# Optimization experiments

Measured on AMD Instinct MI355X. Metric: run time of the kernel, lower is better.

The kernel has to match this reference:

```python
import jax, jax.numpy as jnp
import numpy as np

N_NODES = 50000
N_EDGES = 600000
IN_DIM = 128
HID = 64
HEADS = 4
NEG_SLOPE = 0.2


def _glorot(key, shape):
    fan_in, fan_out = shape[0], shape[-1]
    lim = jnp.sqrt(6.0 / (fan_in + fan_out))
    return jax.random.uniform(key, shape, jnp.float32, -lim, lim)


def setup_inputs() -> dict:
    key = jax.random.key(0)
    ks = jax.random.split(key, 16)
    x = jax.random.normal(ks[0], (N_NODES, IN_DIM), jnp.float32)
    edge_index = jax.random.randint(ks[1], (2, N_EDGES), 0, N_NODES, jnp.int32)
    # GAT layer 1: in=128 -> heads=4, out=64, concat -> 256
    W1 = _glorot(ks[2], (IN_DIM, HEADS * HID))
    a_src1 = _glorot(ks[3], (HEADS, HID))
    a_dst1 = _glorot(ks[4], (HEADS, HID))
    b1 = jnp.zeros((HEADS * HID,), jnp.float32)
    # GAT layer 2: in=256 -> heads=1, out=64, no concat
    W2 = _glorot(ks[5], (HEADS * HID, 1 * HID))
    a_src2 = _glorot(ks[6], (1, HID))
    a_dst2 = _glorot(ks[7], (1, HID))
    b2 = jnp.zeros((HID,), jnp.float32)
    # classifier: Linear(64,32) -> ReLU -> Dropout(eval: identity) -> Linear(32,2)
    Wc1 = _glorot(ks[8], (HID, 32))
    bc1 = jnp.zeros((32,), jnp.float32)
    Wc2 = _glorot(ks[9], (32, 2))
    bc2 = jnp.zeros((2,), jnp.float32)
    return {"x": x, "edge_index": edge_index,
            "W1": W1, "a_src1": a_src1, "a_dst1": a_dst1, "b1": b1,
            "W2": W2, "a_src2": a_src2, "a_dst2": a_dst2, "b2": b2,
            "Wc1": Wc1, "bc1": bc1, "Wc2": Wc2, "bc2": bc2}


def _gat_conv(x, src, dst, W, a_src, a_dst, b, heads, out_ch, concat):
    N = x.shape[0]
    h = (x @ W).reshape(N, heads, out_ch)          # [N,H,C]
    alpha_s = jnp.sum(h * a_src, axis=-1)          # [N,H]
    alpha_d = jnp.sum(h * a_dst, axis=-1)          # [N,H]
    e = jax.nn.leaky_relu(alpha_s[src] + alpha_d[dst], NEG_SLOPE)  # [E,H]
    # segment softmax over edges grouped by destination node
    m = jax.ops.segment_max(e, dst, num_segments=N)                # [N,H]
    ex = jnp.exp(e - m[dst])
    denom = jax.ops.segment_sum(ex, dst, num_segments=N)           # [N,H]
    alpha = ex / (denom[dst] + 1e-16)                              # [E,H]
    msg = h[src] * alpha[:, :, None]                               # [E,H,C]
    out = jax.ops.segment_sum(msg, dst, num_segments=N)            # [N,H,C]
    out = out.reshape(N, heads * out_ch) if concat else out.mean(axis=1)
    return out + b


def reference(x, edge_index, W1, a_src1, a_dst1, b1, W2, a_src2, a_dst2, b2,
              Wc1, bc1, Wc2, bc2):
    N = x.shape[0]
    # PyG GATConv default add_self_loops=True (same augmented edge set both layers)
    loops = jnp.arange(N, dtype=edge_index.dtype)
    src = jnp.concatenate([edge_index[0], loops])
    dst = jnp.concatenate([edge_index[1], loops])
    h = _gat_conv(x, src, dst, W1, a_src1, a_dst1, b1, HEADS, HID, True)
    h = jax.nn.relu(h)
    h = _gat_conv(h, src, dst, W2, a_src2, a_dst2, b2, 1, HID, False)
    h = jax.nn.relu(h)
    h = jax.nn.relu(h @ Wc1 + bc1)   # Dropout(0.2) is identity in eval mode
    return h @ Wc2 + bc2
```

## Files before the change

kernel.cpp:

```cpp
#include <hip/hip_runtime.h>
#include <hip/hip_fp16.h>

#define N_NODES 50000
#define N_EDGESx 600000
#define E_TOT   (N_EDGESx + N_NODES)
#define NEG_SLOPE 0.2f

typedef _Float16 f16x4 __attribute__((ext_vector_type(4)));
typedef float f32x4 __attribute__((ext_vector_type(4)));

__device__ __forceinline__ float lrelu(float x) { return x > 0.f ? x : NEG_SLOPE * x; }

__global__ __launch_bounds__(256) void count_k(const int* __restrict__ ei,
                                               int* __restrict__ counts) {
    int i = blockIdx.x * 256 + threadIdx.x;
    if (i >= E_TOT) return;
    int dst = (i < N_EDGESx) ? ei[N_EDGESx + i] : (i - N_EDGESx);
    atomicAdd(&counts[dst], 1);
}

__global__ __launch_bounds__(1024) void scanA(const int* __restrict__ counts,
                                              int* __restrict__ offs,
                                              int* __restrict__ chunks, int N) {
    __shared__ int sdata[1024];
    int t = threadIdx.x;
    int g = blockIdx.x * 1024 + t;
    int v = (g < N) ? counts[g] : 0;
    sdata[t] = v;
    __syncthreads();
    for (int off = 1; off < 1024; off <<= 1) {
        int x = (t >= off) ? sdata[t - off] : 0;
        __syncthreads();
        sdata[t] += x;
        __syncthreads();
    }
    int incl = sdata[t];
    if (g < N) offs[g] = incl - v;
    if (t == 1023) chunks[blockIdx.x] = incl;
}

__global__ void scanB(int* chunks, int nch) {
    int lane = threadIdx.x & 63;
    int orig = (lane < nch) ? chunks[lane] : 0;
    int v = orig;
#pragma unroll
    for (int off = 1; off < 64; off <<= 1) {
        int u = __shfl_up(v, off);
        if (lane >= off) v += u;
    }
    if (lane < nch) chunks[lane] = v - orig;
}

__global__ __launch_bounds__(1024) void scanC(int* __restrict__ offs,
                                              const int* __restrict__ chunks, int N) {
    int g = blockIdx.x * 1024 + threadIdx.x;
    if (g < N) offs[g] += chunks[blockIdx.x];
}

__global__ __launch_bounds__(256) void scatter_k(const int* __restrict__ ei,
                                                 const int* __restrict__ offs,
                                                 int* __restrict__ cursor,
                                                 int* __restrict__ edge_src) {
    int i = blockIdx.x * 256 + threadIdx.x;
    if (i >= E_TOT) return;
    int src, dst;
    if (i < N_EDGESx) { src = ei[i]; dst = ei[N_EDGESx + i]; }
    else              { src = dst = i - N_EDGESx; }
    int pos = atomicAdd(&cursor[dst], 1);
    edge_src[offs[dst] + pos] = src;
}

__global__ __launch_bounds__(256) void prepBoth_k(const float* __restrict__ W1,
                                                  const float* __restrict__ W2,
                                                  _Float16* __restrict__ Bt1,
                                                  _Float16* __restrict__ Bt2) {
    int b = blockIdx.x;
    if (b < 32) {
        constexpr int K = 128, N = 256;
        int q = b * 256 + threadIdx.x;
        int n = q & (N - 1);
        int k4 = q / N;
        f16x4 v;
#pragma unroll
        for (int i = 0; i < 4; ++i)
            v[i] = (_Float16)W1[(size_t)(k4 * 4 + i) * N + n];
        int idx = n * K + (((k4 >> 1) ^ (n & 15)) << 3) + ((k4 & 1) << 2);
        *(f16x4*)&Bt1[idx] = v;
    } else {
        constexpr int K = 256, N = 64;
        int q = (b - 32) * 256 + threadIdx.x;
        int n = q & (N - 1);
        int k4 = q / N;
        f16x4 v;
#pragma unroll
        for (int i = 0; i < 4; ++i) {
            int kg = k4 * 4 + i;
            int krow = (kg & 3) * 64 + (kg >> 2);
            v[i] = (_Float16)W2[(size_t)krow * N + n];
        }
        int idx = n * K + (((k4 >> 1) ^ (n & 15)) << 3) + ((k4 & 1) << 2);
        *(f16x4*)&Bt2[idx] = v;
    }
}

template<int K, int N, int CPW, typename AT, int CPERM, int ALPHA>
__global__ __launch_bounds__(256, 2) void gemm_mfma(const AT* __restrict__ A,
                                                    const _Float16* __restrict__ Bt,
                                                    _Float16* __restrict__ C,
                                                    const float* __restrict__ asrc,
                                                    const float* __restrict__ adst,
                                                    float* __restrict__ as_o,
                                                    float* __restrict__ ad_o, int M) {
    __shared__ __align__(16) _Float16 Ah[64 * K];
    __shared__ __align__(16) _Float16 Bh[N * K];
    const int t = threadIdx.x;
    const int row0 = blockIdx.x * 64;

#pragma unroll
    for (int q = t; q < 64 * K / 4; q += 256) {
        int r = q / (K / 4);
        int k4 = q % (K / 4);
        f16x4 v;
        int grow = row0 + r;
        if (grow < M) {
            if constexpr (sizeof(AT) == 4) {
                float4 f = *(const float4*)(A + (size_t)grow * K + k4 * 4);
                v[0] = (_Float16)f.x; v[1] = (_Float16)f.y;
                v[2] = (_Float16)f.z; v[3] = (_Float16)f.w;
            } else {
                v = *(const f16x4*)(A + (size_t)grow * K + k4 * 4);
            }
        } else {
            v[0] = v[1] = v[2] = v[3] = (_Float16)0.f;
        }
        int idx = r * K + (((k4 >> 1) ^ (r & 15)) << 3) + ((k4 & 1) << 2);
        *(f16x4*)&Ah[idx] = v;
    }
#pragma unroll
    for (int q = t; q < N * K / 8; q += 256)
        ((uint4*)Bh)[q] = ((const uint4*)Bt)[q];
    __syncthreads();

    const int w = t >> 6;
    const int l = t & 63;
    const int lr = l & 15;
    const int g = l >> 4;

    f32x4 acc[4][CPW];
#pragma unroll
    for (int mt = 0; mt < 4; ++mt)
#pragma unroll
        for (int nt = 0; nt < CPW; ++nt)
            acc[mt][nt] = (f32x4){0.f, 0.f, 0.f, 0.f};

#pragma unroll
    for (int ks = 0; ks < K / 16; ++ks) {
        int k = ks * 16 + g * 4;
        f16x4 a[4], b[CPW];
#pragma unroll
        for (int mt = 0; mt < 4; ++mt) {
            int r = mt * 16 + lr;
            a[mt] = *(const f16x4*)&Ah[r * K + (((k >> 3) ^ (r & 15)) << 3) + (k & 7)];
        }
#pragma unroll
        for (int nt = 0; nt < CPW; ++nt) {
            int n = (w * CPW + nt) * 16 + lr;
            b[nt] = *(const f16x4*)&Bh[n * K + (((k >> 3) ^ (n & 15)) << 3) + (k & 7)];
        }
#pragma unroll
        for (int mt = 0; mt < 4; ++mt)
#pragma unroll
            for (int nt = 0; nt < CPW; ++nt)
                acc[mt][nt] = __builtin_amdgcn_mfma_f32_16x16x16f16(a[mt], b[nt],
                                                                   acc[mt][nt], 0, 0, 0);
    }

    if constexpr (CPERM) {
        float* A_s  = (float*)Ah;
        float* A_d  = A_s + 256;
        float* psum = A_d + 256;
        __syncthreads();
        _Float16* Cs = Bh;
#pragma unroll
        for (int mt = 0; mt < 4; ++mt)
#pragma unroll
            for (int q = 0; q < 4; ++q) {
                int row = mt * 16 + g * 4 + q;
#pragma unroll
                for (int nt = 0; nt < CPW; ++nt) {
                    int gcol = (w * CPW + nt) * 16 + lr;
                    int ocol = ((gcol & 63) << 2) | (gcol >> 6);
                    Cs[row * N + ocol] = (_Float16)acc[mt][nt][q];
                }
            }
        if constexpr (ALPHA == 1) { A_s[t] = asrc[t]; A_d[t] = adst[t]; }
        __syncthreads();
#pragma unroll
        for (int q = t; q < 64 * N / 8; q += 256) {
            int row = q / (N / 8);
            int c8 = q % (N / 8);
            int grow = row0 + row;
            if (grow < M)
                *(float4*)(C + (size_t)grow * N + c8 * 8) =
                    *(const float4*)&Cs[row * N + c8 * 8];
        }
        if constexpr (ALPHA == 1) {
            int row = t & 63, qr = t >> 6;
            float s[4] = {}, d[4] = {};
#pragma unroll
            for (int j = 0; j < 16; ++j) {
                int c = qr * 16 + j;
                union { uint2 u; __half h[4]; } U;
                U.u = *(const uint2*)&Cs[row * 256 + c * 4];
#pragma unroll
                for (int h = 0; h < 4; ++h) {
                    float f = __half2float(U.h[h]);
                    s[h] += f * A_s[h * 64 + c];
                    d[h] += f * A_d[h * 64 + c];
                }
            }
            float* ps = psum + (row * 4 + qr) * 8;
#pragma unroll
            for (int h = 0; h < 4; ++h) { ps[h] = s[h]; ps[4 + h] = d[h]; }
            __syncthreads();
            if (t < 64 && row0 + t < M) {
                float4 S = make_float4(0.f, 0.f, 0.f, 0.f);
                float4 D = make_float4(0.f, 0.f, 0.f, 0.f);
#pragma unroll
                for (int q2 = 0; q2 < 4; ++q2) {
                    float* ps2 = psum + (t * 4 + q2) * 8;
                    S.x += ps2[0]; S.y += ps2[1]; S.z += ps2[2]; S.w += ps2[3];
                    D.x += ps2[4]; D.y += ps2[5]; D.z += ps2[6]; D.w += ps2[7];
                }
                *(float4*)(as_o + (size_t)(row0 + t) * 4) = S;
                *(float4*)(ad_o + (size_t)(row0 + t) * 4) = D;
            }
        }
    } else {
#pragma unroll
        for (int mt = 0; mt < 4; ++mt)
#pragma unroll
            for (int q = 0; q < 4; ++q) {
                int grow = row0 + mt * 16 + g * 4 + q;
                if (grow >= M) continue;
#pragma unroll
                for (int nt = 0; nt < CPW; ++nt) {
                    int gcol = (w * CPW + nt) * 16 + lr;
                    C[(size_t)grow * N + gcol] = (_Float16)acc[mt][nt][q];
                }
            }
        if constexpr (ALPHA == 2) {
            __half* Ch  = (__half*)Ah;
            float*  A_s = (float*)(Ch + 64 * 64);
            float*  A_d = A_s + 64;
            float*  psum = A_d + 64;
            __syncthreads();
#pragma unroll
            for (int mt = 0; mt < 4; ++mt)
#pragma unroll
                for (int q = 0; q < 4; ++q) {
                    int row = mt * 16 + g * 4 + q;
                    Ch[row * 64 + w * 16 + lr] = __float2half(acc[mt][0][q]);
                }
            if (t < 64) { A_s[t] = asrc[t]; A_d[t] = adst[t]; }
            __syncthreads();
            int row = t & 63, qr = t >> 6;
            float s = 0.f, d = 0.f;
#pragma unroll
            for (int j = 0; j < 16; ++j) {
                int c = qr * 16 + j;
                float f = __half2float(Ch[row * 64 + c]);
                s += f * A_s[c];
                d += f * A_d[c];
            }
            psum[(row * 4 + qr) * 2]     = s;
            psum[(row * 4 + qr) * 2 + 1] = d;
            __syncthreads();
            if (t < 64 && row0 + t < M) {
                float S = 0.f, D = 0.f;
#pragma unroll
                for (int q2 = 0; q2 < 4; ++q2) {
                    S += psum[(t * 4 + q2) * 2];
                    D += psum[(t * 4 + q2) * 2 + 1];
                }
                as_o[row0 + t] = S;
                ad_o[row0 + t] = D;
            }
        }
    }
}

__global__ __launch_bounds__(256) void stats1w_k(const int* __restrict__ edge_src,
                                                 const float* __restrict__ as1,
                                                 const float* __restrict__ ad1,
                                                 const int* __restrict__ offs,
                                                 const int* __restrict__ counts,
                                                 __half* __restrict__ w4, int N) {
    int lane = threadIdx.x & 63;
    int n = blockIdx.x * 4 + (threadIdx.x >> 6);
    if (n >= N) return;
    int start = offs[n];
    int end = start + counts[n];
    int h4 = lane & 3;
    float4 ad = *(const float4*)(ad1 + (size_t)n * 4);
    float adh = h4 == 0 ? ad.x : h4 == 1 ? ad.y : h4 == 2 ? ad.z : ad.w;
    float m = -1e30f, s = 0.f;
    for (int p = start + (lane >> 2); p < end; p += 16) {
        float e = lrelu(as1[(size_t)edge_src[p] * 4 + h4] + adh);
        float nm = fmaxf(m, e);
        s = s * __expf(m - nm) + __expf(e - nm);
        m = nm;
    }
#pragma unroll
    for (int i = 0; i < 4; ++i) {
        int msk = 4 << i;
        float om = __shfl_xor(m, msk);
        float os = __shfl_xor(s, msk);
        float nm = fmaxf(m, om);
        s = s * __expf(m - nm) + os * __expf(om - nm);
        m = nm;
    }
    float rcp = 1.f / (s + 1e-16f);
    float4 mh = make_float4(__shfl(m, 0), __shfl(m, 1), __shfl(m, 2), __shfl(m, 3));
    float4 rs = make_float4(__shfl(rcp, 0), __shfl(rcp, 1), __shfl(rcp, 2), __shfl(rcp, 3));
    for (int p = start + lane; p < end; p += 64) {
        float4 a = *(const float4*)(as1 + (size_t)edge_src[p] * 4);
        union { uint2 u; __half h[4]; } W;
        W.h[0] = __float2half(__expf(lrelu(a.x + ad.x) - mh.x) * rs.x);
        W.h[1] = __float2half(__expf(lrelu(a.y + ad.y) - mh.y) * rs.y);
        W.h[2] = __float2half(__expf(lrelu(a.z + ad.z) - mh.z) * rs.z);
        W.h[3] = __float2half(__expf(lrelu(a.w + ad.w) - mh.w) * rs.w);
        *(uint2*)(w4 + (size_t)p * 4) = W.u;
    }
}

__global__ __launch_bounds__(256) void stats2w_k(const int* __restrict__ edge_src,
                                                 const float* __restrict__ as2,
                                                 const float* __restrict__ ad2,
                                                 const int* __restrict__ offs,
                                                 const int* __restrict__ counts,
                                                 __half* __restrict__ w2, int N) {
    int lane = threadIdx.x & 63;
    int n = blockIdx.x * 4 + (threadIdx.x >> 6);
    if (n >= N) return;
    int start = offs[n];
    int end = start + counts[n];
    float adn = ad2[n];
    float m = -1e30f, s = 0.f;
    for (int p = start + lane; p < end; p += 64) {
        float e = lrelu(as2[edge_src[p]] + adn);
        float nm = fmaxf(m, e);
        s = s * __expf(m - nm) + __expf(e - nm);
        m = nm;
    }
#pragma unroll
    for (int i = 0; i < 6; ++i) {
        int msk = 1 << i;
        float om = __shfl_xor(m, msk);
        float os = __shfl_xor(s, msk);
        float nm = fmaxf(m, om);
        s = s * __expf(m - nm) + os * __expf(om - nm);
        m = nm;
    }
    float rn = 1.f / (s + 1e-16f);
    for (int p = start + lane; p < end; p += 64)
        w2[p] = __float2half(__expf(lrelu(as2[edge_src[p]] + adn) - m) * rn);
}

__global__ __launch_bounds__(256) void agg1_k(const __half* __restrict__ h1,
                                              const __half* __restrict__ w4,
                                              const int* __restrict__ edge_src,
                                              const int* __restrict__ offs,
                                              const int* __restrict__ counts,
                                              const float* __restrict__ b1,
                                              __half* __restrict__ out1, int N) {
    int lane = threadIdx.x & 63;
    int n = blockIdx.x * 4 + (threadIdx.x >> 6);
    if (n >= N) return;
    int start = offs[n];
    int end = start + counts[n];
    float acc0 = 0.f, acc1 = 0.f, acc2 = 0.f, acc3 = 0.f;
    int p = start;
    for (; p + 7 < end; p += 8) {
        int s[8]; uint2 hw[8], ww[8];
#pragma unroll
        for (int i = 0; i < 8; ++i) s[i] = edge_src[p + i];
#pragma unroll
        for (int i = 0; i < 8; ++i) ww[i] = *(const uint2*)(w4 + (size_t)(p + i) * 4);
#pragma unroll
        for (int i = 0; i < 8; ++i) hw[i] = *(const uint2*)(h1 + (size_t)s[i] * 256 + lane * 4);
#pragma unroll
        for (int i = 0; i < 8; ++i) {
            union { uint2 u; __half h[4]; } U, W;
            U.u = hw[i]; W.u = ww[i];
            acc0 += __half2float(U.h[0]) * __half2float(W.h[0]);
            acc1 += __half2float(U.h[1]) * __half2float(W.h[1]);
            acc2 += __half2float(U.h[2]) * __half2float(W.h[2]);
            acc3 += __half2float(U.h[3]) * __half2float(W.h[3]);
        }
    }
    for (; p < end; ++p) {
        int s0 = edge_src[p];
        union { uint2 u; __half h[4]; } U0, W0;
        W0.u = *(const uint2*)(w4 + (size_t)p * 4);
        U0.u = *(const uint2*)(h1 + (size_t)s0 * 256 + lane * 4);
        acc0 += __half2float(U0.h[0]) * __half2float(W0.h[0]);
        acc1 += __half2float(U0.h[1]) * __half2float(W0.h[1]);
        acc2 += __half2float(U0.h[2]) * __half2float(W0.h[2]);
        acc3 += __half2float(U0.h[3]) * __half2float(W0.h[3]);
    }
    union { uint2 u; __half h[4]; } O;
    O.h[0] = __float2half(fmaxf(acc0 + b1[lane], 0.f));
    O.h[1] = __float2half(fmaxf(acc1 + b1[64 + lane], 0.f));
    O.h[2] = __float2half(fmaxf(acc2 + b1[128 + lane], 0.f));
    O.h[3] = __float2half(fmaxf(acc3 + b1[192 + lane], 0.f));
    *(uint2*)(out1 + (size_t)n * 256 + lane * 4) = O.u;
}

__global__ __launch_bounds__(256) void agg2_k(const __half* __restrict__ h2,
                                              const __half* __restrict__ w2,
                                              const int* __restrict__ edge_src,
                                              const int* __restrict__ offs,
                                              const int* __restrict__ counts,
                                              const float* __restrict__ b2,
                                              __half* __restrict__ out2, int N) {
    int l32 = threadIdx.x & 31;
    int n = blockIdx.x * 8 + (threadIdx.x >> 5);
    if (n >= N) return;
    int start = offs[n];
    int end = start + counts[n];
    float ax = 0.f, ay = 0.f;
    int p = start;
    for (; p + 7 < end; p += 8) {
        int s[8]; __half wv8[8]; __half2 hv8[8];
#pragma unroll
        for (int i = 0; i < 8; ++i) s[i] = edge_src[p + i];
#pragma unroll
        for (int i = 0; i < 8; ++i) wv8[i] = w2[p + i];
#pragma unroll
        for (int i = 0; i < 8; ++i)
            hv8[i] = *(const __half2*)(h2 + (size_t)s[i] * 64 + l32 * 2);
#pragma unroll
        for (int i = 0; i < 8; ++i) {
            float w = __half2float(wv8[i]);
            float2 f = __half22float2(hv8[i]);
            ax += f.x * w; ay += f.y * w;
        }
    }
    for (; p < end; ++p) {
        float w = __half2float(w2[p]);
        float2 f = __half22float2(*(const __half2*)(h2 + (size_t)edge_src[p] * 64 + l32 * 2));
        ax += f.x * w; ay += f.y * w;
    }
    __half2 o;
    o.x = __float2half(fmaxf(ax + b2[l32 * 2], 0.f));
    o.y = __float2half(fmaxf(ay + b2[l32 * 2 + 1], 0.f));
    *(__half2*)(out2 + (size_t)n * 64 + l32 * 2) = o;
}

__global__ __launch_bounds__(256) void cls_k(const __half* __restrict__ hin,
                                             const float* __restrict__ Wc1,
                                             const float* __restrict__ bc1,
                                             const float* __restrict__ Wc2,
                                             const float* __restrict__ bc2,
                                             float* __restrict__ out, int N) {
    __shared__ float W1s[64 * 32];
    __shared__ float W2s[64];
    __shared__ float b1s[32];
    __shared__ float b2s[2];
    __shared__ float z[8][33];
    int t = threadIdx.x;
    for (int i = t; i < 2048; i += 256) W1s[i] = Wc1[i];
    if (t < 64) W2s[t] = Wc2[t];
    if (t < 32) b1s[t] = bc1[t];
    if (t < 2)  b2s[t] = bc2[t];
    __syncthreads();
    int nl = t >> 5, j = t & 31;
    int n = blockIdx.x * 8 + nl;
    float acc = b1s[j];
    if (n < N) {
        const __half* hr = hin + (size_t)n * 64;
#pragma unroll 8
        for (int l = 0; l < 64; ++l) acc += __half2float(hr[l]) * W1s[l * 32 + j];
    }
    z[nl][j] = fmaxf(acc, 0.f);
    __syncthreads();
    if (j < 2 && n < N) {
        float o = b2s[j];
#pragma unroll
        for (int q = 0; q < 32; ++q) o += z[nl][q] * W2s[q * 2 + j];
        out[(size_t)n * 2 + j] = o;
    }
}

extern "C" void kernel_launch(void* const* d_in, const int* in_sizes, int n_in,
                              void* d_out, int out_size, void* d_ws, size_t ws_size,
                              hipStream_t stream) {
    const float* x      = (const float*)d_in[0];
    const int*   ei     = (const int*)d_in[1];
    const float* W1     = (const float*)d_in[2];
    const float* a_src1 = (const float*)d_in[3];
    const float* a_dst1 = (const float*)d_in[4];
    const float* b1     = (const float*)d_in[5];
    const float* W2     = (const float*)d_in[6];
    const float* a_src2 = (const float*)d_in[7];
    const float* a_dst2 = (const float*)d_in[8];
    const float* b2     = (const float*)d_in[9];
    const float* Wc1    = (const float*)d_in[10];
    const float* bc1    = (const float*)d_in[11];
    const float* Wc2    = (const float*)d_in[12];
    const float* bc2    = (const float*)d_in[13];

    char* ws = (char*)d_ws;
    size_t off = 0;
    auto alloc = [&](size_t bytes) -> void* {
        void* p = ws + off;
        off += (bytes + 255) & ~(size_t)255;
        return p;
    };
    int*       counts   = (int*)alloc((size_t)N_NODES * 4);
    int*       cursor   = (int*)alloc((size_t)N_NODES * 4);
    int*       offs     = (int*)alloc((size_t)N_NODES * 4);
    int*       chunks   = (int*)alloc(256);
    int*       edge_src = (int*)alloc((size_t)E_TOT * 4);
    float*     as1      = (float*)alloc((size_t)N_NODES * 16);
    float*     ad1      = (float*)alloc((size_t)N_NODES * 16);
    float*     as2      = (float*)alloc((size_t)N_NODES * 4);
    float*     ad2      = (float*)alloc((size_t)N_NODES * 4);
    __half*    w4       = (__half*)alloc((size_t)E_TOT * 8);
    _Float16*  Bt1      = (_Float16*)alloc((size_t)256 * 128 * 2);
    _Float16*  Bt2      = (_Float16*)alloc((size_t)64 * 256 * 2);
    __half*    h1h      = (__half*)alloc((size_t)N_NODES * 256 * 2);
    __half*    out1h    = (__half*)alloc((size_t)N_NODES * 256 * 2);
    __half*    out2h    = (__half*)alloc((size_t)N_NODES * 64 * 2);
    __half*    h2h  = h1h;
    __half*    w2b  = w4;

    const int EB = (E_TOT + 255) / 256;
    const int NB4 = (N_NODES + 3) / 4;
    const int NB8 = (N_NODES + 7) / 8;
    const int NCH = (N_NODES + 1023) / 1024;
    const int MB = (N_NODES + 63) / 64;

    hipMemsetAsync(counts, 0, (char*)cursor - (char*)counts + (size_t)N_NODES * 4, stream);

    count_k<<<EB, 256, 0, stream>>>(ei, counts);
    scanA<<<NCH, 1024, 0, stream>>>(counts, offs, chunks, N_NODES);
    scanB<<<1, 64, 0, stream>>>(chunks, NCH);
    scanC<<<NCH, 1024, 0, stream>>>(offs, chunks, N_NODES);
    scatter_k<<<EB, 256, 0, stream>>>(ei, offs, cursor, edge_src);

    prepBoth_k<<<48, 256, 0, stream>>>(W1, W2, Bt1, Bt2);

    gemm_mfma<128, 256, 4, float, 1, 1><<<MB, 256, 0, stream>>>(
        x, Bt1, (_Float16*)h1h, a_src1, a_dst1, as1, ad1, N_NODES);
    stats1w_k<<<NB4, 256, 0, stream>>>(edge_src, as1, ad1, offs, counts, w4, N_NODES);
    agg1_k<<<NB4, 256, 0, stream>>>(h1h, w4, edge_src, offs, counts, b1, out1h, N_NODES);

    gemm_mfma<256, 64, 1, _Float16, 0, 2><<<MB, 256, 0, stream>>>(
        (const _Float16*)out1h, Bt2, (_Float16*)h2h, a_src2, a_dst2, as2, ad2, N_NODES);
    stats2w_k<<<NB4, 256, 0, stream>>>(edge_src, as2, ad2, offs, counts, w2b, N_NODES);
    agg2_k<<<NB8, 256, 0, stream>>>(h2h, w2b, edge_src, offs, counts, b2, out2h, N_NODES);

    cls_k<<<N_NODES / 8, 256, 0, stream>>>(out2h, Wc1, bc1, Wc2, bc2, (float*)d_out, N_NODES);
}
```

Measured before the change: 257.2 us.

## Use 16-lane groups per node in stats/agg kernels and fuse prep with count

Each node in stats1w, stats2w and agg2 is now handled by 16 lanes instead of 64 or 32. The average degree is about 13, so most lanes in the wider groups sat idle. The shuffle reductions are shortened to match, and agg2 now loads 4 halfs per lane with uint2 accesses. The weight prep kernel is merged into the edge-count kernel to remove one launch. The trade-off is more serial loop iterations for high-degree nodes.

```diff
diff --git a/kernel.cpp b/kernel.cpp
--- a/kernel.cpp
+++ b/kernel.cpp
@@ -11,12 +11,44 @@
 
 __device__ __forceinline__ float lrelu(float x) { return x > 0.f ? x : NEG_SLOPE * x; }
 
-__global__ __launch_bounds__(256) void count_k(const int* __restrict__ ei,
-                                               int* __restrict__ counts) {
-    int i = blockIdx.x * 256 + threadIdx.x;
-    if (i >= E_TOT) return;
-    int dst = (i < N_EDGESx) ? ei[N_EDGESx + i] : (i - N_EDGESx);
-    atomicAdd(&counts[dst], 1);
+__global__ __launch_bounds__(256) void prepcnt_k(const float* __restrict__ W1,
+                                                 const float* __restrict__ W2,
+                                                 _Float16* __restrict__ Bt1,
+                                                 _Float16* __restrict__ Bt2,
+                                                 const int* __restrict__ ei,
+                                                 int* __restrict__ counts) {
+    int b = blockIdx.x;
+    if (b < 32) {
+        constexpr int K = 128, N = 256;
+        int q = b * 256 + threadIdx.x;
+        int n = q & (N - 1);
+        int k4 = q / N;
+        f16x4 v;
+#pragma unroll
+        for (int i = 0; i < 4; ++i)
+            v[i] = (_Float16)W1[(size_t)(k4 * 4 + i) * N + n];
+        int idx = n * K + (((k4 >> 1) ^ (n & 15)) << 3) + ((k4 & 1) << 2);
+        *(f16x4*)&Bt1[idx] = v;
+    } else if (b < 48) {
+        constexpr int K = 256, N = 64;
+        int q = (b - 32) * 256 + threadIdx.x;
+        int n = q & (N - 1);
+        int k4 = q / N;
+        f16x4 v;
+#pragma unroll
+        for (int i = 0; i < 4; ++i) {
+            int kg = k4 * 4 + i;
+            int krow = (kg & 3) * 64 + (kg >> 2);
+            v[i] = (_Float16)W2[(size_t)krow * N + n];
+        }
+        int idx = n * K + (((k4 >> 1) ^ (n & 15)) << 3) + ((k4 & 1) << 2);
+        *(f16x4*)&Bt2[idx] = v;
+    } else {
+        int i = (b - 48) * 256 + threadIdx.x;
+        if (i >= E_TOT) return;
+        int dst = (i < N_EDGESx) ? ei[N_EDGESx + i] : (i - N_EDGESx);
+        atomicAdd(&counts[dst], 1);
+    }
 }
 
 __global__ __launch_bounds__(1024) void scanA(const int* __restrict__ counts,
@@ -70,39 +102,6 @@
     edge_src[offs[dst] + pos] = src;
 }
 
-__global__ __launch_bounds__(256) void prepBoth_k(const float* __restrict__ W1,
-                                                  const float* __restrict__ W2,
-                                                  _Float16* __restrict__ Bt1,
-                                                  _Float16* __restrict__ Bt2) {
-    int b = blockIdx.x;
-    if (b < 32) {
-        constexpr int K = 128, N = 256;
-        int q = b * 256 + threadIdx.x;
-        int n = q & (N - 1);
-        int k4 = q / N;
-        f16x4 v;
-#pragma unroll
-        for (int i = 0; i < 4; ++i)
-            v[i] = (_Float16)W1[(size_t)(k4 * 4 + i) * N + n];
-        int idx = n * K + (((k4 >> 1) ^ (n & 15)) << 3) + ((k4 & 1) << 2);
-        *(f16x4*)&Bt1[idx] = v;
-    } else {
-        constexpr int K = 256, N = 64;
-        int q = (b - 32) * 256 + threadIdx.x;
-        int n = q & (N - 1);
-        int k4 = q / N;
-        f16x4 v;
-#pragma unroll
-        for (int i = 0; i < 4; ++i) {
-            int kg = k4 * 4 + i;
-            int krow = (kg & 3) * 64 + (kg >> 2);
-            v[i] = (_Float16)W2[(size_t)krow * N + n];
-        }
-        int idx = n * K + (((k4 >> 1) ^ (n & 15)) << 3) + ((k4 & 1) << 2);
-        *(f16x4*)&Bt2[idx] = v;
-    }
-}
-
 template<int K, int N, int CPW, typename AT, int CPERM, int ALPHA>
 __global__ __launch_bounds__(256, 2) void gemm_mfma(const AT* __restrict__ A,
                                                     const _Float16* __restrict__ Bt,
@@ -296,23 +295,24 @@
                                                  const int* __restrict__ offs,
                                                  const int* __restrict__ counts,
                                                  __half* __restrict__ w4, int N) {
-    int lane = threadIdx.x & 63;
-    int n = blockIdx.x * 4 + (threadIdx.x >> 6);
+    int t = threadIdx.x;
+    int l16 = t & 15;
+    int n = blockIdx.x * 16 + (t >> 4);
     if (n >= N) return;
     int start = offs[n];
     int end = start + counts[n];
-    int h4 = lane & 3;
+    int h4 = l16 & 3;
     float4 ad = *(const float4*)(ad1 + (size_t)n * 4);
     float adh = h4 == 0 ? ad.x : h4 == 1 ? ad.y : h4 == 2 ? ad.z : ad.w;
     float m = -1e30f, s = 0.f;
-    for (int p = start + (lane >> 2); p < end; p += 16) {
+    for (int p = start + (l16 >> 2); p < end; p += 4) {
         float e = lrelu(as1[(size_t)edge_src[p] * 4 + h4] + adh);
         float nm = fmaxf(m, e);
         s = s * __expf(m - nm) + __expf(e - nm);
         m = nm;
     }
 #pragma unroll
-    for (int i = 0; i < 4; ++i) {
+    for (int i = 0; i < 2; ++i) {
         int msk = 4 << i;
         float om = __shfl_xor(m, msk);
         float os = __shfl_xor(s, msk);
@@ -321,9 +321,10 @@
         m = nm;
     }
     float rcp = 1.f / (s + 1e-16f);
-    float4 mh = make_float4(__shfl(m, 0), __shfl(m, 1), __shfl(m, 2), __shfl(m, 3));
-    float4 rs = make_float4(__shfl(rcp, 0), __shfl(rcp, 1), __shfl(rcp, 2), __shfl(rcp, 3));
-    for (int p = start + lane; p < end; p += 64) {
+    int gb = (t & 63) & ~15;
+    float4 mh = make_float4(__shfl(m, gb), __shfl(m, gb + 1), __shfl(m, gb + 2), __shfl(m, gb + 3));
+    float4 rs = make_float4(__shfl(rcp, gb), __shfl(rcp, gb + 1), __shfl(rcp, gb + 2), __shfl(rcp, gb + 3));
+    for (int p = start + l16; p < end; p += 16) {
         float4 a = *(const float4*)(as1 + (size_t)edge_src[p] * 4);
         union { uint2 u; __half h[4]; } W;
         W.h[0] = __float2half(__expf(lrelu(a.x + ad.x) - mh.x) * rs.x);
@@ -340,21 +341,22 @@
                                                  const int* __restrict__ offs,
                                                  const int* __restrict__ counts,
                                                  __half* __restrict__ w2, int N) {
-    int lane = threadIdx.x & 63;
-    int n = blockIdx.x * 4 + (threadIdx.x >> 6);
+    int t = threadIdx.x;
+    int l16 = t & 15;
+    int n = blockIdx.x * 16 + (t >> 4);
     if (n >= N) return;
     int start = offs[n];
     int end = start + counts[n];
     float adn = ad2[n];
     float m = -1e30f, s = 0.f;
-    for (int p = start + lane; p < end; p += 64) {
+    for (int p = start + l16; p < end; p += 16) {
         float e = lrelu(as2[edge_src[p]] + adn);
         float nm = fmaxf(m, e);
         s = s * __expf(m - nm) + __expf(e - nm);
         m = nm;
     }
 #pragma unroll
-    for (int i = 0; i < 6; ++i) {
+    for (int i = 0; i < 4; ++i) {
         int msk = 1 << i;
         float om = __shfl_xor(m, msk);
         float os = __shfl_xor(s, msk);
@@ -363,7 +365,7 @@
         m = nm;
     }
     float rn = 1.f / (s + 1e-16f);
-    for (int p = start + lane; p < end; p += 64)
+    for (int p = start + l16; p < end; p += 16)
         w2[p] = __float2half(__expf(lrelu(as2[edge_src[p]] + adn) - m) * rn);
 }
 
@@ -424,38 +426,50 @@
                                               const int* __restrict__ counts,
                                               const float* __restrict__ b2,
                                               __half* __restrict__ out2, int N) {
-    int l32 = threadIdx.x & 31;
-    int n = blockIdx.x * 8 + (threadIdx.x >> 5);
+    int t = threadIdx.x;
+    int l16 = t & 15;
+    int n = blockIdx.x * 16 + (t >> 4);
     if (n >= N) return;
     int start = offs[n];
     int end = start + counts[n];
-    float ax = 0.f, ay = 0.f;
+    float a0 = 0.f, a1 = 0.f, a2 = 0.f, a3 = 0.f;
     int p = start;
     for (; p + 7 < end; p += 8) {
-        int s[8]; __half wv8[8]; __half2 hv8[8];
+        int s[8]; __half wv8[8]; uint2 hv8[8];
 #pragma unroll
         for (int i = 0; i < 8; ++i) s[i] = edge_src[p + i];
 #pragma unroll
         for (int i = 0; i < 8; ++i) wv8[i] = w2[p + i];
 #pragma unroll
         for (int i = 0; i < 8; ++i)
-            hv8[i] = *(const __half2*)(h2 + (size_t)s[i] * 64 + l32 * 2);
+            hv8[i] = *(const uint2*)(h2 + (size_t)s[i] * 64 + l16 * 4);
 #pragma unroll
         for (int i = 0; i < 8; ++i) {
+            union { uint2 u; __half h[4]; } U;
+            U.u = hv8[i];
             float w = __half2float(wv8[i]);
-            float2 f = __half22float2(hv8[i]);
-            ax += f.x * w; ay += f.y * w;
+            a0 += __half2float(U.h[0]) * w;
+            a1 += __half2float(U.h[1]) * w;
+            a2 += __half2float(U.h[2]) * w;
+            a3 += __half2float(U.h[3]) * w;
         }
     }
     for (; p < end; ++p) {
+        int s0 = edge_src[p];
+        union { uint2 u; __half h[4]; } U;
+        U.u = *(const uint2*)(h2 + (size_t)s0 * 64 + l16 * 4);
         float w = __half2float(w2[p]);
-        float2 f = __half22float2(*(const __half2*)(h2 + (size_t)edge_src[p] * 64 + l32 * 2));
-        ax += f.x * w; ay += f.y * w;
-    }
-    __half2 o;
-    o.x = __float2half(fmaxf(ax + b2[l32 * 2], 0.f));
-    o.y = __float2half(fmaxf(ay + b2[l32 * 2 + 1], 0.f));
-    *(__half2*)(out2 + (size_t)n * 64 + l32 * 2) = o;
+        a0 += __half2float(U.h[0]) * w;
+        a1 += __half2float(U.h[1]) * w;
+        a2 += __half2float(U.h[2]) * w;
+        a3 += __half2float(U.h[3]) * w;
+    }
+    union { uint2 u; __half h[4]; } O;
+    O.h[0] = __float2half(fmaxf(a0 + b2[l16 * 4],     0.f));
+    O.h[1] = __float2half(fmaxf(a1 + b2[l16 * 4 + 1], 0.f));
+    O.h[2] = __float2half(fmaxf(a2 + b2[l16 * 4 + 2], 0.f));
+    O.h[3] = __float2half(fmaxf(a3 + b2[l16 * 4 + 3], 0.f));
+    *(uint2*)(out2 + (size_t)n * 64 + l16 * 4) = O.u;
 }
 
 __global__ __launch_bounds__(256) void cls_k(const __half* __restrict__ hin,
@@ -538,29 +552,27 @@
 
     const int EB = (E_TOT + 255) / 256;
     const int NB4 = (N_NODES + 3) / 4;
-    const int NB8 = (N_NODES + 7) / 8;
+    const int NB16 = (N_NODES + 15) / 16;
     const int NCH = (N_NODES + 1023) / 1024;
     const int MB = (N_NODES + 63) / 64;
 
     hipMemsetAsync(counts, 0, (char*)cursor - (char*)counts + (size_t)N_NODES * 4, stream);
 
-    count_k<<<EB, 256, 0, stream>>>(ei, counts);
+    prepcnt_k<<<48 + EB, 256, 0, stream>>>(W1, W2, Bt1, Bt2, ei, counts);
     scanA<<<NCH, 1024, 0, stream>>>(counts, offs, chunks, N_NODES);
     scanB<<<1, 64, 0, stream>>>(chunks, NCH);
     scanC<<<NCH, 1024, 0, stream>>>(offs, chunks, N_NODES);
     scatter_k<<<EB, 256, 0, stream>>>(ei, offs, cursor, edge_src);
 
-    prepBoth_k<<<48, 256, 0, stream>>>(W1, W2, Bt1, Bt2);
-
     gemm_mfma<128, 256, 4, float, 1, 1><<<MB, 256, 0, stream>>>(
         x, Bt1, (_Float16*)h1h, a_src1, a_dst1, as1, ad1, N_NODES);
-    stats1w_k<<<NB4, 256, 0, stream>>>(edge_src, as1, ad1, offs, counts, w4, N_NODES);
+    stats1w_k<<<NB16, 256, 0, stream>>>(edge_src, as1, ad1, offs, counts, w4, N_NODES);
     agg1_k<<<NB4, 256, 0, stream>>>(h1h, w4, edge_src, offs, counts, b1, out1h, N_NODES);
 
     gemm_mfma<256, 64, 1, _Float16, 0, 2><<<MB, 256, 0, stream>>>(
         (const _Float16*)out1h, Bt2, (_Float16*)h2h, a_src2, a_dst2, as2, ad2, N_NODES);
-    stats2w_k<<<NB4, 256, 0, stream>>>(edge_src, as2, ad2, offs, counts, w2b, N_NODES);
-    agg2_k<<<NB8, 256, 0, stream>>>(h2h, w2b, edge_src, offs, counts, b2, out2h, N_NODES);
+    stats2w_k<<<NB16, 256, 0, stream>>>(edge_src, as2, ad2, offs, counts, w2b, N_NODES);
+    agg2_k<<<NB16, 256, 0, stream>>>(h2h, w2b, edge_src, offs, counts, b2, out2h, N_NODES);
 
     cls_k<<<N_NODES / 8, 256, 0, stream>>>(out2h, Wc1, bc1, Wc2, bc2, (float*)d_out, N_NODES);
 }
```

New measurement: 235.0 us. 8.6% less time.
